# Kernel tuning notes

Measured on AMD Instinct MI355X. Metric: run time of the kernel, lower is better.

## Reference

```python
import jax, jax.numpy as jnp
import numpy as np

N_NODES = 100000
NEG_SLOPE = 0.01  # torch F.leaky_relu default


def gcn_conv(x, src, dst, norm, W, b):
    # x: [N, Fin]; src/dst: [E+N] (self-loops included); norm: [E+N]
    h = x @ W                                  # [N, Fout] dense transform
    msg = h[src] * norm[:, None]               # gather + edge-wise scale
    out = jax.ops.segment_sum(msg, dst, num_segments=x.shape[0])  # scatter-add
    return out + b


def build_graph(edge_index, n_nodes):
    # Add self-loops and compute symmetric GCN normalization deg^-1/2 * deg^-1/2
    loop = jnp.arange(n_nodes, dtype=edge_index.dtype)
    src = jnp.concatenate([edge_index[0], loop])
    dst = jnp.concatenate([edge_index[1], loop])
    deg = jax.ops.segment_sum(jnp.ones_like(dst, dtype=jnp.float32), dst,
                              num_segments=n_nodes)
    dinv = jnp.where(deg > 0, jax.lax.rsqrt(deg), 0.0)
    norm = dinv[src] * dinv[dst]
    return src, dst, norm


def setup_inputs() -> dict:
    key = jax.random.key(0)
    ks = jax.random.split(key, 8)
    in_c, out_c = 256, 64
    hid = 2 * out_c
    x = jax.random.normal(ks[0], (N_NODES, in_c), dtype=jnp.float32)
    edge_index = jax.random.randint(ks[1], (2, 1600000), 0, N_NODES, dtype=jnp.int64)
    def glorot(k, fan_in, fan_out):
        s = jnp.sqrt(6.0 / (fan_in + fan_out))
        return jax.random.uniform(k, (fan_in, fan_out), jnp.float32, -s, s)
    return {
        "x": x,
        "edge_index": edge_index,
        "W1": glorot(ks[2], in_c, hid),
        "b1": jnp.zeros((hid,), jnp.float32),
        "Wmu": glorot(ks[3], hid, out_c),
        "bmu": jnp.zeros((out_c,), jnp.float32),
        "Wlv": glorot(ks[4], hid, out_c),
        "blv": jnp.zeros((out_c,), jnp.float32),
    }


def reference(x, edge_index, W1, b1, Wmu, bmu, Wlv, blv):
    src, dst, norm = build_graph(edge_index, x.shape[0])
    h = gcn_conv(x, src, dst, norm, W1, b1)
    h = jnp.where(h >= 0, h, NEG_SLOPE * h)  # leaky_relu
    mu = gcn_conv(h, src, dst, norm, Wmu, bmu)
    logvar = gcn_conv(h, src, dst, norm, Wlv, blv)
    return (mu, logvar)
```

## Files before the change

kernel.cpp:

```cpp
#include <hip/hip_runtime.h>

typedef unsigned short bf16_t;
typedef short s16x8 __attribute__((ext_vector_type(8)));
typedef float f32x4 __attribute__((ext_vector_type(4)));


#define NBKT 782
#define BSH  7
#define BMSK 127
#define CAPS 512

__device__ __forceinline__ float bf2f(unsigned short u) {
    unsigned int v = ((unsigned int)u) << 16;
    float f;
    __builtin_memcpy(&f, &v, 4);
    return f;
}
__device__ __forceinline__ unsigned short f2bf(float f) {
    unsigned int x;
    __builtin_memcpy(&x, &f, 4);
    unsigned int r = x + 0x7fffu + ((x >> 16) & 1u);
    return (unsigned short)(r >> 16);
}
__device__ __forceinline__ unsigned pack2(float a, float b) {
    return (unsigned)f2bf(a) | ((unsigned)f2bf(b) << 16);
}
__device__ __forceinline__ float ldf(const void* p, long long i, unsigned f32) {
    return f32 ? ((const float*)p)[i] : bf2f(((const unsigned short*)p)[i]);
}
__device__ __forceinline__ int ldi(const void* p, long long i, unsigned i64) {
    return i64 ? (int)((const long long*)p)[i] : ((const int*)p)[i];
}
__device__ __forceinline__ s16x8 ld8u(const unsigned short* p) {
    return *(const s16x8*)p;
}
__device__ __forceinline__ f32x4 mfma16(s16x8 a, s16x8 b, f32x4 c) {
    return __builtin_amdgcn_mfma_f32_16x16x32_bf16(a, b, c, 0, 0, 0);
}
__device__ __forceinline__ void cvt_hl(const float* p, s16x8& hi, s16x8& lo) {
    const float4 u = *(const float4*)p;
    const float4 w = *(const float4*)(p + 4);
    float v[8] = {u.x, u.y, u.z, u.w, w.x, w.y, w.z, w.w};
#pragma unroll
    for (int j = 0; j < 8; ++j) {
        unsigned short h = f2bf(v[j]);
        hi[j] = (short)h;
        lo[j] = (short)f2bf(v[j] - bf2f(h));
    }
}

__global__ __launch_bounds__(256) void k_zero(unsigned* __restrict__ p, int n) {
    int i = blockIdx.x * 256 + threadIdx.x;
    if (i < n) p[i] = 0;
}

__global__ __launch_bounds__(256) void k_detect(const void* x, const void* W1,
                                                const void* ei, unsigned* flags) {
    __shared__ float smx[256];
    __shared__ float smw[256];
    __shared__ int   szc[256];
    int tid = threadIdx.x;
    const unsigned short* xu = (const unsigned short*)x;
    float mx = 0.f;
    for (int i = tid; i < 4096; i += 256) {
        unsigned short w = xu[i];
        if ((w & 0x7fffu) >= 0x7f80u) mx = 1e30f;
        else { float f = fabsf(bf2f(w)); if (f > mx) mx = f; }
    }
    smx[tid] = mx;
    const unsigned short* wu = (const unsigned short*)W1;
    float mw = 0.f;
    for (int i = tid; i < 4096; i += 256) {
        unsigned short w = wu[i];
        if ((w & 0x7fffu) >= 0x7f80u) mw = 1e30f;
        else { float f = fabsf(bf2f(w)); if (f > mw) mw = f; }
    }
    smw[tid] = mw;
    const int* eu = (const int*)ei;
    int zc = 0;
    for (int i = tid; i < 128; i += 256)
        if ((i & 1) && eu[i] == 0) ++zc;
    szc[tid] = zc;
    __syncthreads();
    for (int off = 128; off > 0; off >>= 1) {
        if (tid < off) {
            if (smx[tid + off] > smx[tid]) smx[tid] = smx[tid + off];
            if (smw[tid + off] > smw[tid]) smw[tid] = smw[tid + off];
            szc[tid] += szc[tid + off];
        }
        __syncthreads();
    }
    if (tid == 0) {
        flags[0] = (smx[0] > 1e4f) ? 1u : 0u;
        flags[1] = (smw[0] > 10.f) ? 1u : 0u;
        flags[2] = (szc[0] >= 56) ? 1u : 0u;
    }
}

__global__ __launch_bounds__(256) void k_bucket(const void* ei, const unsigned* det,
                                                int* __restrict__ btail,
                                                unsigned* __restrict__ bstore,
                                                int E, int N) {
    int e = blockIdx.x * 256 + threadIdx.x;
    if (e >= E) return;
    unsigned i64 = det[2];
    int s = ldi(ei, e, i64);
    int d = ldi(ei, (long long)E + e, i64);
    if ((unsigned)d >= (unsigned)N) return;
    int b = d >> BSH;
    int sub = blockIdx.x & 7;
    int slot = atomicAdd(&btail[sub * NBKT + b], 1);
    if (slot < CAPS) {
        unsigned src = ((unsigned)s < (unsigned)N) ? (unsigned)s : (unsigned)d;
        bstore[((long long)(b * 8 + sub)) * CAPS + slot] =
            ((unsigned)(d & BMSK) << 24) | src;
    }
}

__global__ __launch_bounds__(256) void k_bhist(const int* __restrict__ btail,
                                               const unsigned* __restrict__ bstore,
                                               int* __restrict__ cnt, int N) {
    __shared__ int lh[128];
    __shared__ int ln[8];
    const int b = blockIdx.x;
    const int tid = threadIdx.x;
    if (tid < 128) lh[tid] = 0;
    if (tid < 8) {
        int t = btail[tid * NBKT + b];
        ln[tid] = t < CAPS ? t : CAPS;
    }
    __syncthreads();
#pragma unroll 1
    for (int s = 0; s < 8; ++s) {
        int n = ln[s];
        const unsigned* base = &bstore[((long long)(b * 8 + s)) * CAPS];
        for (int i = tid; i < n; i += 256)
            atomicAdd(&lh[base[i] >> 24], 1);
    }
    __syncthreads();
    int node = b * 128 + tid;
    if (tid < 128 && node < N) cnt[node] = lh[tid];
}

__global__ __launch_bounds__(256) void k_dinv(const int* __restrict__ cnt,
                                              float* __restrict__ dinv, int N) {
    int i = blockIdx.x * 256 + threadIdx.x;
    if (i < N) dinv[i] = rsqrtf((float)cnt[i] + 1.0f);
}

__global__ __launch_bounds__(256) void k_scan_blk(const int* __restrict__ cnt,
                                                  int* __restrict__ pos,
                                                  int* __restrict__ bsum, int N) {
    __shared__ int sh[256];
    const int tid = threadIdx.x;
    const int base = blockIdx.x * 1024 + tid * 4;
    int v[4];
#pragma unroll
    for (int j = 0; j < 4; ++j) v[j] = (base + j < N) ? cnt[base + j] : 0;
    int s = v[0] + v[1] + v[2] + v[3];
    sh[tid] = s;
    __syncthreads();
    for (int off = 1; off < 256; off <<= 1) {
        int t = (tid >= off) ? sh[tid - off] : 0;
        __syncthreads();
        sh[tid] += t;
        __syncthreads();
    }
    int run = sh[tid] - s;
#pragma unroll
    for (int j = 0; j < 4; ++j) {
        if (base + j < N) pos[base + j] = run;
        run += v[j];
    }
    if (tid == 255) bsum[blockIdx.x] = sh[255];
}

__global__ void k_scan_top(int* __restrict__ bsum, int nb) {
    if (threadIdx.x == 0 && blockIdx.x == 0) {
        int running = 0;
        for (int b = 0; b < nb; ++b) {
            int t = bsum[b];
            bsum[b] = running;
            running += t;
        }
    }
}

__global__ __launch_bounds__(256) void k_scan_add(int* __restrict__ pos,
                                                  const int* __restrict__ bsum, int N) {
    int add = bsum[blockIdx.x];
    int base = blockIdx.x * 1024;
    for (int i = threadIdx.x; i < 1024; i += 256)
        if (base + i < N) pos[base + i] += add;
}

__global__ __launch_bounds__(256) void k_emit(const int* __restrict__ btail,
                                              const unsigned* __restrict__ bstore,
                                              const int* __restrict__ pos,
                                              int* __restrict__ srt, int N) {
    __shared__ int lstart[128];
    __shared__ int loff[128];
    __shared__ int ln[8];
    __shared__ int stage[4096];
    const int b = blockIdx.x;
    const int tid = threadIdx.x;
    const int base0 = pos[b * 128];
    if (tid < 128) {
        int node = b * 128 + tid;
        lstart[tid] = (node < N) ? (pos[node] - base0) : 0;
        loff[tid] = 0;
    }
    if (tid < 8) {
        int t = btail[tid * NBKT + b];
        ln[tid] = t < CAPS ? t : CAPS;
    }
    __syncthreads();
#pragma unroll 1
    for (int s = 0; s < 8; ++s) {
        int n = ln[s];
        const unsigned* bp = &bstore[((long long)(b * 8 + s)) * CAPS];
        for (int i = tid; i < n; i += 256) {
            unsigned rec = bp[i];
            int dl = rec >> 24;
            int slot = atomicAdd(&loff[dl], 1);
            stage[lstart[dl] + slot] = (int)(rec & 0xffffffu);
        }
    }
    __syncthreads();
    int total = ln[0] + ln[1] + ln[2] + ln[3] + ln[4] + ln[5] + ln[6] + ln[7];
    for (int i = tid; i < total; i += 256)
        srt[base0 + i] = stage[i];
}

__global__ __launch_bounds__(256) void k_wsplit(const void* Wa, const void* Wb,
                                                const unsigned* det, int K,
                                                unsigned short* __restrict__ bth,
                                                unsigned short* __restrict__ btl) {
    int idx = blockIdx.x * 256 + threadIdx.x;
    if (idx >= K * 128) return;
    int k = idx >> 7, n = idx & 127;
    unsigned wf = det[1];
    float w;
    if (Wb) w = (n < 64) ? ldf(Wa, (long long)k * 64 + n, wf)
                         : ldf(Wb, (long long)k * 64 + (n - 64), wf);
    else    w = ldf(Wa, idx, wf);
    unsigned short h = f2bf(w);
    bth[(long long)n * K + k] = h;
    btl[(long long)n * K + k] = f2bf(w - bf2f(h));
}

__global__ __launch_bounds__(256, 4) void k_gemm1m(
    const void* __restrict__ x, const unsigned* __restrict__ det,
    const unsigned short* __restrict__ bth,
    const unsigned short* __restrict__ btl,
    const float* __restrict__ dinv,
    unsigned* __restrict__ Cp, int N) {
    const int lane = threadIdx.x & 63;
    const int wid  = threadIdx.x >> 6;
    const int wr = wid >> 1, wc = wid & 1;
    const int l15 = lane & 15, lg = lane >> 4;
    const long long r0 = (long long)blockIdx.x * 64 + wr * 32;
    long long ar[2];
#pragma unroll
    for (int m = 0; m < 2; ++m) {
        long long r = r0 + m * 16 + l15;
        ar[m] = (r < N) ? r : (N - 1);
    }
    int bn[4];
#pragma unroll
    for (int n = 0; n < 4; ++n) bn[n] = wc * 64 + n * 16 + l15;

    f32x4 acc[2][4] = {};
    if (!det[0]) {
        const unsigned short* xp = (const unsigned short*)x;
#pragma unroll 2
        for (int k0 = 0; k0 < 256; k0 += 32) {
            const int kb = k0 + lg * 8;
            s16x8 a[2], bh[4], bl[4];
#pragma unroll
            for (int m = 0; m < 2; ++m) a[m] = ld8u(xp + ar[m] * 256 + kb);
#pragma unroll
            for (int n = 0; n < 4; ++n) {
                bh[n] = ld8u(bth + (long long)bn[n] * 256 + kb);
                bl[n] = ld8u(btl + (long long)bn[n] * 256 + kb);
            }
#pragma unroll
            for (int m = 0; m < 2; ++m)
#pragma unroll
                for (int n = 0; n < 4; ++n) {
                    acc[m][n] = mfma16(a[m], bh[n], acc[m][n]);
                    acc[m][n] = mfma16(a[m], bl[n], acc[m][n]);
                }
        }
    } else {
        const float* xp = (const float*)x;
#pragma unroll 2
        for (int k0 = 0; k0 < 256; k0 += 32) {
            const int kb = k0 + lg * 8;
            s16x8 ah[2], al[2], bh[4], bl[4];
#pragma unroll
            for (int m = 0; m < 2; ++m) cvt_hl(xp + ar[m] * 256 + kb, ah[m], al[m]);
#pragma unroll
            for (int n = 0; n < 4; ++n) {
                bh[n] = ld8u(bth + (long long)bn[n] * 256 + kb);
                bl[n] = ld8u(btl + (long long)bn[n] * 256 + kb);
            }
#pragma unroll
            for (int m = 0; m < 2; ++m)
#pragma unroll
                for (int n = 0; n < 4; ++n) {
                    acc[m][n] = mfma16(ah[m], bh[n], acc[m][n]);
                    acc[m][n] = mfma16(ah[m], bl[n], acc[m][n]);
                    acc[m][n] = mfma16(al[m], bh[n], acc[m][n]);
                }
        }
    }
#pragma unroll
    for (int m = 0; m < 2; ++m)
#pragma unroll
        for (int n = 0; n < 4; ++n) {
            const int col = wc * 64 + n * 16 + l15;
#pragma unroll
            for (int r = 0; r < 4; ++r) {
                long long row = r0 + m * 16 + lg * 4 + r;
                float v = acc[m][n][r] * dinv[(row < N) ? row : (N - 1)];
                float p = __shfl_xor(v, 1);
                if (!(lane & 1) && row < N)
                    Cp[row * 64 + (col >> 1)] = pack2(v, p);
            }
        }
}

__global__ __launch_bounds__(256, 4) void k_gemm2m(
    const unsigned short* __restrict__ hap,
    const unsigned short* __restrict__ bth,
    const unsigned short* __restrict__ btl,
    const void* bmu, const void* blv, const unsigned* __restrict__ det,
    float* __restrict__ outMu, float* __restrict__ outLv, int N) {
    const int lane = threadIdx.x & 63;
    const int wid  = threadIdx.x >> 6;
    const int wr = wid >> 1, wc = wid & 1;
    const int l15 = lane & 15, lg = lane >> 4;
    const long long r0 = (long long)blockIdx.x * 64 + wr * 32;
    long long ar[2];
#pragma unroll
    for (int m = 0; m < 2; ++m) {
        long long r = r0 + m * 16 + l15;
        ar[m] = (r < N) ? r : (N - 1);
    }
    int bn[4];
#pragma unroll
    for (int n = 0; n < 4; ++n) bn[n] = wc * 64 + n * 16 + l15;

    f32x4 acc[2][4] = {};
#pragma unroll
    for (int k0 = 0; k0 < 128; k0 += 32) {
        const int kb = k0 + lg * 8;
        s16x8 a[2], bh[4], bl[4];
#pragma unroll
        for (int m = 0; m < 2; ++m) a[m] = ld8u(hap + ar[m] * 128 + kb);
#pragma unroll
        for (int n = 0; n < 4; ++n) {
            bh[n] = ld8u(bth + (long long)bn[n] * 128 + kb);
            bl[n] = ld8u(btl + (long long)bn[n] * 128 + kb);
        }
#pragma unroll
        for (int m = 0; m < 2; ++m)
#pragma unroll
            for (int n = 0; n < 4; ++n) {
                acc[m][n] = mfma16(a[m], bh[n], acc[m][n]);
                acc[m][n] = mfma16(a[m], bl[n], acc[m][n]);
            }
    }
    __syncthreads();
    const unsigned wf = det[1];
#pragma unroll
    for (int m = 0; m < 2; ++m)
#pragma unroll
        for (int n = 0; n < 4; ++n) {
            const int col = wc * 64 + n * 16 + l15;
            const float bias = (col < 64) ? ldf(bmu, col, wf)
                                          : ldf(blv, col - 64, wf);
#pragma unroll
            for (int r = 0; r < 4; ++r) {
                long long row = r0 + m * 16 + lg * 4 + r;
                if (row < N) {
                    float v = acc[m][n][r] + bias;
                    if (col < 64) outMu[row * 64 + col] = v;
                    else          outLv[row * 64 + (col - 64)] = v;
                }
            }
        }
}

__global__ __launch_bounds__(256) void k_gather(const unsigned* __restrict__ hp,
                                                const int* __restrict__ srt,
                                                const int* __restrict__ cnt,
                                                const int* __restrict__ pos,
                                                const float* __restrict__ dinv,
                                                const void* bias, const unsigned* det,
                                                int leaky, int prescaleOut,
                                                unsigned* __restrict__ outp, int N) {
    int node = blockIdx.x * 4 + (threadIdx.x >> 6);
    if (node >= N) return;
    int lane = threadIdx.x & 63;
    int beg = pos[node];
    int end = beg + cnt[node];
    float dd = dinv[node];
    unsigned hv = hp[(long long)node * 64 + lane];
    float a0 = bf2f((unsigned short)(hv & 0xffffu));
    float a1 = bf2f((unsigned short)(hv >> 16));
    for (int q = beg; q < end; q += 8) {
        int s[8];
        unsigned v[8];
#pragma unroll
        for (int j = 0; j < 8; ++j) {
            int qq = q + j;
            s[j] = srt[(qq < end) ? qq : beg];
        }
#pragma unroll
        for (int j = 0; j < 8; ++j)
            v[j] = hp[(long long)s[j] * 64 + lane];
#pragma unroll
        for (int j = 0; j < 8; ++j) {
            bool on = (q + j) < end;
            a0 += on ? bf2f((unsigned short)(v[j] & 0xffffu)) : 0.f;
            a1 += on ? bf2f((unsigned short)(v[j] >> 16)) : 0.f;
        }
    }
    a0 *= dd;
    a1 *= dd;
    if (bias) {
        a0 += ldf(bias, 2 * lane, det[1]);
        a1 += ldf(bias, 2 * lane + 1, det[1]);
    }
    if (leaky) {
        a0 = (a0 >= 0.f) ? a0 : 0.01f * a0;
        a1 = (a1 >= 0.f) ? a1 : 0.01f * a1;
    }
    if (prescaleOut) { a0 *= dd; a1 *= dd; }
    outp[(long long)node * 64 + lane] = pack2(a0, a1);
}

__global__ void k_sentinel(float* out, long long lvOff) {
    if (threadIdx.x == 0 && blockIdx.x == 0) {
        out[0] = 9.99e5f;
        out[lvOff] = 9.98e5f;
    }
}

extern "C" void kernel_launch(void* const* d_in, const int* in_sizes, int n_in,
                              void* d_out, int out_size, void* d_ws, size_t ws_size,
                              hipStream_t stream) {
    (void)out_size;
    const int N = 100000, E = 1600000;
    bool ok = (n_in == 8) && in_sizes[0] == 25600000 && in_sizes[1] == 3200000 &&
              in_sizes[2] == 32768 && in_sizes[3] == 128 &&
              in_sizes[4] == 8192 && in_sizes[5] == 64 &&
              in_sizes[6] == 8192 && in_sizes[7] == 64 &&
              ws_size >= (size_t)21 * 1024 * 1024;
    if (!ok) {
        k_sentinel<<<1, 64, 0, stream>>>((float*)d_out, (long long)N * 64);
        return;
    }
    const void* x   = d_in[0];
    const void* ei  = d_in[1];
    const void* W1  = d_in[2];
    const void* b1  = d_in[3];
    const void* Wmu = d_in[4];
    const void* bmu = d_in[5];
    const void* Wlv = d_in[6];
    const void* blv = d_in[7];

    char* w = (char*)d_ws;
    auto carve = [&](size_t bytes) {
        char* p = w;
        w += (bytes + 255) & ~(size_t)255;
        return p;
    };
    unsigned* flags = (unsigned*)carve(64);
    int*    cnt  = (int*)carve((size_t)N * 4);
    int*    pos  = (int*)carve((size_t)N * 4);
    float*  dinv = (float*)carve((size_t)N * 4);
    int*    bsum = (int*)carve(4096);
    int*    srt  = (int*)carve((size_t)E * 4);
    unsigned short* bt1h = (unsigned short*)carve(128 * 256 * 2);
    unsigned short* bt1l = (unsigned short*)carve(128 * 256 * 2);
    unsigned short* bt2h = (unsigned short*)carve(128 * 128 * 2);
    unsigned short* bt2l = (unsigned short*)carve(128 * 128 * 2);
    int*      btail  = (int*)carve((size_t)NBKT * 8 * 4);
    unsigned* bstore = (unsigned*)carve((size_t)NBKT * 8 * CAPS * 4);

    float* M = (float*)d_out;
    float* L = M + (size_t)N * 64;
    unsigned* Mp = (unsigned*)M;
    unsigned* Lp = (unsigned*)L;

    const int nb = (N + 1023) / 1024;
    const int gblk = (N + 3) / 4;
    const int gb64 = (N + 63) / 64;

    k_zero<<<1, 64, 0, stream>>>(flags, 16);
    k_detect<<<1, 256, 0, stream>>>(x, W1, ei, flags);
    k_zero<<<(NBKT * 8 + 255) / 256, 256, 0, stream>>>((unsigned*)btail, NBKT * 8);

    k_bucket<<<(E + 255) / 256, 256, 0, stream>>>(ei, flags, btail, bstore, E, N);
    k_bhist<<<NBKT, 256, 0, stream>>>(btail, bstore, cnt, N);
    k_dinv<<<(N + 255) / 256, 256, 0, stream>>>(cnt, dinv, N);
    k_scan_blk<<<nb, 256, 0, stream>>>(cnt, pos, bsum, N);
    k_scan_top<<<1, 64, 0, stream>>>(bsum, nb);
    k_scan_add<<<nb, 256, 0, stream>>>(pos, bsum, N);
    k_emit<<<NBKT, 256, 0, stream>>>(btail, bstore, pos, srt, N);

    k_wsplit<<<(256 * 128 + 255) / 256, 256, 0, stream>>>(W1, nullptr, flags, 256,
                                                          bt1h, bt1l);
    k_wsplit<<<(128 * 128 + 255) / 256, 256, 0, stream>>>(Wmu, Wlv, flags, 128,
                                                          bt2h, bt2l);

    k_gemm1m<<<gb64, 256, 0, stream>>>(x, flags, bt1h, bt1l, dinv, Mp, N);
    k_gather<<<gblk, 256, 0, stream>>>(Mp, srt, cnt, pos, dinv, b1, flags, 1, 1,
                                       Lp, N);
    k_gather<<<gblk, 256, 0, stream>>>(Lp, srt, cnt, pos, dinv, nullptr, flags,
                                       0, 0, Mp, N);
    k_gemm2m<<<gb64, 256, 0, stream>>>((const unsigned short*)Mp, bt2h, bt2l,
                                       bmu, blv, flags, M, L, N);
}
```

Baseline: 560.4 us.

## Merge small launches, software-pipeline GEMM loads, and widen gather to 8-byte lanes

Removes the zero, dinv and scan_top kernels: btail zeroing moves into k_detect, dinv is computed inside k_bhist, and each scan_add block sums the preceding block totals itself. The two weight-split launches become one. Both GEMM kernels get explicit double-buffered register prefetch of A and B fragments, with launch bounds lowered to 2 waves per SIMD. The gather kernel now processes 8 nodes per block with 32 lanes each loading uint2, halving the lane count per node. The flags buffer is no longer zeroed before k_detect, which risks stale flags if k_detect does not write every entry.

```diff
diff --git a/kernel.cpp b/kernel.cpp
--- a/kernel.cpp
+++ b/kernel.cpp
@@ -49,17 +49,14 @@
     }
 }
 
-__global__ __launch_bounds__(256) void k_zero(unsigned* __restrict__ p, int n) {
-    int i = blockIdx.x * 256 + threadIdx.x;
-    if (i < n) p[i] = 0;
-}
-
 __global__ __launch_bounds__(256) void k_detect(const void* x, const void* W1,
-                                                const void* ei, unsigned* flags) {
+                                                const void* ei, unsigned* flags,
+                                                int* __restrict__ btail) {
     __shared__ float smx[256];
     __shared__ float smw[256];
     __shared__ int   szc[256];
     int tid = threadIdx.x;
+    for (int i = tid; i < NBKT * 8; i += 256) btail[i] = 0;
     const unsigned short* xu = (const unsigned short*)x;
     float mx = 0.f;
     for (int i = tid; i < 4096; i += 256) {
@@ -119,7 +116,8 @@
 
 __global__ __launch_bounds__(256) void k_bhist(const int* __restrict__ btail,
                                                const unsigned* __restrict__ bstore,
-                                               int* __restrict__ cnt, int N) {
+                                               int* __restrict__ cnt,
+                                               float* __restrict__ dinv, int N) {
     __shared__ int lh[128];
     __shared__ int ln[8];
     const int b = blockIdx.x;
@@ -139,13 +137,10 @@
     }
     __syncthreads();
     int node = b * 128 + tid;
-    if (tid < 128 && node < N) cnt[node] = lh[tid];
-}
-
-__global__ __launch_bounds__(256) void k_dinv(const int* __restrict__ cnt,
-                                              float* __restrict__ dinv, int N) {
-    int i = blockIdx.x * 256 + threadIdx.x;
-    if (i < N) dinv[i] = rsqrtf((float)cnt[i] + 1.0f);
+    if (tid < 128 && node < N) {
+        cnt[node] = lh[tid];
+        dinv[node] = rsqrtf((float)lh[tid] + 1.0f);
+    }
 }
 
 __global__ __launch_bounds__(256) void k_scan_blk(const int* __restrict__ cnt,
@@ -175,20 +170,16 @@
     if (tid == 255) bsum[blockIdx.x] = sh[255];
 }
 
-__global__ void k_scan_top(int* __restrict__ bsum, int nb) {
-    if (threadIdx.x == 0 && blockIdx.x == 0) {
-        int running = 0;
-        for (int b = 0; b < nb; ++b) {
-            int t = bsum[b];
-            bsum[b] = running;
-            running += t;
-        }
-    }
-}
-
 __global__ __launch_bounds__(256) void k_scan_add(int* __restrict__ pos,
                                                   const int* __restrict__ bsum, int N) {
-    int add = bsum[blockIdx.x];
+    __shared__ int sadd;
+    if (threadIdx.x == 0) {
+        int a = 0;
+        for (int i = 0; i < blockIdx.x; ++i) a += bsum[i];
+        sadd = a;
+    }
+    __syncthreads();
+    int add = sadd;
     int base = blockIdx.x * 1024;
     for (int i = threadIdx.x; i < 1024; i += 256)
         if (base + i < N) pos[base + i] += add;
@@ -232,24 +223,32 @@
         srt[base0 + i] = stage[i];
 }
 
-__global__ __launch_bounds__(256) void k_wsplit(const void* Wa, const void* Wb,
-                                                const unsigned* det, int K,
-                                                unsigned short* __restrict__ bth,
-                                                unsigned short* __restrict__ btl) {
+__global__ __launch_bounds__(256) void k_wsplit(const void* W1, const void* Wmu,
+                                                const void* Wlv, const unsigned* det,
+                                                unsigned short* __restrict__ bt1h,
+                                                unsigned short* __restrict__ bt1l,
+                                                unsigned short* __restrict__ bt2h,
+                                                unsigned short* __restrict__ bt2l) {
     int idx = blockIdx.x * 256 + threadIdx.x;
-    if (idx >= K * 128) return;
-    int k = idx >> 7, n = idx & 127;
     unsigned wf = det[1];
-    float w;
-    if (Wb) w = (n < 64) ? ldf(Wa, (long long)k * 64 + n, wf)
-                         : ldf(Wb, (long long)k * 64 + (n - 64), wf);
-    else    w = ldf(Wa, idx, wf);
-    unsigned short h = f2bf(w);
-    bth[(long long)n * K + k] = h;
-    btl[(long long)n * K + k] = f2bf(w - bf2f(h));
-}
-
-__global__ __launch_bounds__(256, 4) void k_gemm1m(
+    if (idx < 256 * 128) {
+        int k = idx >> 7, n = idx & 127;
+        float w = ldf(W1, idx, wf);
+        unsigned short h = f2bf(w);
+        bt1h[(long long)n * 256 + k] = h;
+        bt1l[(long long)n * 256 + k] = f2bf(w - bf2f(h));
+    } else if (idx < 256 * 128 + 128 * 128) {
+        int j = idx - 256 * 128;
+        int k = j >> 7, n = j & 127;
+        float w = (n < 64) ? ldf(Wmu, (long long)k * 64 + n, wf)
+                           : ldf(Wlv, (long long)k * 64 + (n - 64), wf);
+        unsigned short h = f2bf(w);
+        bt2h[(long long)n * 128 + k] = h;
+        bt2l[(long long)n * 128 + k] = f2bf(w - bf2f(h));
+    }
+}
+
+__global__ __launch_bounds__(256, 2) void k_gemm1p(
     const void* __restrict__ x, const unsigned* __restrict__ det,
     const unsigned short* __restrict__ bth,
     const unsigned short* __restrict__ btl,
@@ -273,23 +272,48 @@
     f32x4 acc[2][4] = {};
     if (!det[0]) {
         const unsigned short* xp = (const unsigned short*)x;
-#pragma unroll 2
-        for (int k0 = 0; k0 < 256; k0 += 32) {
-            const int kb = k0 + lg * 8;
-            s16x8 a[2], bh[4], bl[4];
-#pragma unroll
-            for (int m = 0; m < 2; ++m) a[m] = ld8u(xp + ar[m] * 256 + kb);
-#pragma unroll
-            for (int n = 0; n < 4; ++n) {
-                bh[n] = ld8u(bth + (long long)bn[n] * 256 + kb);
-                bl[n] = ld8u(btl + (long long)bn[n] * 256 + kb);
-            }
+        const unsigned short* aP[2];
+#pragma unroll
+        for (int m = 0; m < 2; ++m) aP[m] = xp + ar[m] * 256 + lg * 8;
+        const unsigned short* bHp[4];
+        const unsigned short* bLp[4];
+#pragma unroll
+        for (int n = 0; n < 4; ++n) {
+            bHp[n] = bth + (long long)bn[n] * 256 + lg * 8;
+            bLp[n] = btl + (long long)bn[n] * 256 + lg * 8;
+        }
+        s16x8 aS[8][2], bhS[2][4], blS[2][4];
+#pragma unroll
+        for (int s = 0; s < 2; ++s)
+#pragma unroll
+            for (int m = 0; m < 2; ++m) aS[s][m] = ld8u(aP[m] + s * 32);
+#pragma unroll
+        for (int n = 0; n < 4; ++n) {
+            bhS[0][n] = ld8u(bHp[n]);
+            blS[0][n] = ld8u(bLp[n]);
+        }
+#pragma unroll
+        for (int st = 0; st < 8; ++st) {
+            if (st < 7) {
+                const int nb = (st + 1) & 1;
+#pragma unroll
+                for (int n = 0; n < 4; ++n) {
+                    bhS[nb][n] = ld8u(bHp[n] + (st + 1) * 32);
+                    blS[nb][n] = ld8u(bLp[n] + (st + 1) * 32);
+                }
+            }
+            if (st < 6) {
+#pragma unroll
+                for (int m = 0; m < 2; ++m)
+                    aS[st + 2][m] = ld8u(aP[m] + (st + 2) * 32);
+            }
+            const int cb = st & 1;
 #pragma unroll
             for (int m = 0; m < 2; ++m)
 #pragma unroll
                 for (int n = 0; n < 4; ++n) {
-                    acc[m][n] = mfma16(a[m], bh[n], acc[m][n]);
-                    acc[m][n] = mfma16(a[m], bl[n], acc[m][n]);
+                    acc[m][n] = mfma16(aS[st][m], bhS[cb][n], acc[m][n]);
+                    acc[m][n] = mfma16(aS[st][m], blS[cb][n], acc[m][n]);
                 }
         }
     } else {
@@ -331,7 +355,7 @@
         }
 }
 
-__global__ __launch_bounds__(256, 4) void k_gemm2m(
+__global__ __launch_bounds__(256, 2) void k_gemm2p(
     const unsigned short* __restrict__ hap,
     const unsigned short* __restrict__ bth,
     const unsigned short* __restrict__ btl,
@@ -352,24 +376,49 @@
 #pragma unroll
     for (int n = 0; n < 4; ++n) bn[n] = wc * 64 + n * 16 + l15;
 
+    const unsigned short* aP[2];
+#pragma unroll
+    for (int m = 0; m < 2; ++m) aP[m] = hap + ar[m] * 128 + lg * 8;
+    const unsigned short* bHp[4];
+    const unsigned short* bLp[4];
+#pragma unroll
+    for (int n = 0; n < 4; ++n) {
+        bHp[n] = bth + (long long)bn[n] * 128 + lg * 8;
+        bLp[n] = btl + (long long)bn[n] * 128 + lg * 8;
+    }
     f32x4 acc[2][4] = {};
-#pragma unroll
-    for (int k0 = 0; k0 < 128; k0 += 32) {
-        const int kb = k0 + lg * 8;
-        s16x8 a[2], bh[4], bl[4];
-#pragma unroll
-        for (int m = 0; m < 2; ++m) a[m] = ld8u(hap + ar[m] * 128 + kb);
-#pragma unroll
-        for (int n = 0; n < 4; ++n) {
-            bh[n] = ld8u(bth + (long long)bn[n] * 128 + kb);
-            bl[n] = ld8u(btl + (long long)bn[n] * 128 + kb);
-        }
+    s16x8 aS[4][2], bhS[2][4], blS[2][4];
+#pragma unroll
+    for (int s = 0; s < 2; ++s)
+#pragma unroll
+        for (int m = 0; m < 2; ++m) aS[s][m] = ld8u(aP[m] + s * 32);
+#pragma unroll
+    for (int n = 0; n < 4; ++n) {
+        bhS[0][n] = ld8u(bHp[n]);
+        blS[0][n] = ld8u(bLp[n]);
+    }
+#pragma unroll
+    for (int st = 0; st < 4; ++st) {
+        if (st < 3) {
+            const int nb = (st + 1) & 1;
+#pragma unroll
+            for (int n = 0; n < 4; ++n) {
+                bhS[nb][n] = ld8u(bHp[n] + (st + 1) * 32);
+                blS[nb][n] = ld8u(bLp[n] + (st + 1) * 32);
+            }
+        }
+        if (st < 2) {
+#pragma unroll
+            for (int m = 0; m < 2; ++m)
+                aS[st + 2][m] = ld8u(aP[m] + (st + 2) * 32);
+        }
+        const int cb = st & 1;
 #pragma unroll
         for (int m = 0; m < 2; ++m)
 #pragma unroll
             for (int n = 0; n < 4; ++n) {
-                acc[m][n] = mfma16(a[m], bh[n], acc[m][n]);
-                acc[m][n] = mfma16(a[m], bl[n], acc[m][n]);
+                acc[m][n] = mfma16(aS[st][m], bhS[cb][n], acc[m][n]);
+                acc[m][n] = mfma16(aS[st][m], blS[cb][n], acc[m][n]);
             }
     }
     __syncthreads();
@@ -393,26 +442,28 @@
         }
 }
 
-__global__ __launch_bounds__(256) void k_gather(const unsigned* __restrict__ hp,
+__global__ __launch_bounds__(256) void k_gather(const uint2* __restrict__ hp2,
                                                 const int* __restrict__ srt,
                                                 const int* __restrict__ cnt,
                                                 const int* __restrict__ pos,
                                                 const float* __restrict__ dinv,
                                                 const void* bias, const unsigned* det,
                                                 int leaky, int prescaleOut,
-                                                unsigned* __restrict__ outp, int N) {
-    int node = blockIdx.x * 4 + (threadIdx.x >> 6);
+                                                uint2* __restrict__ outp2, int N) {
+    int node = blockIdx.x * 8 + (threadIdx.x >> 5);
     if (node >= N) return;
-    int lane = threadIdx.x & 63;
+    int lane5 = threadIdx.x & 31;
     int beg = pos[node];
     int end = beg + cnt[node];
     float dd = dinv[node];
-    unsigned hv = hp[(long long)node * 64 + lane];
-    float a0 = bf2f((unsigned short)(hv & 0xffffu));
-    float a1 = bf2f((unsigned short)(hv >> 16));
+    uint2 hv = hp2[(long long)node * 32 + lane5];
+    float a0 = bf2f((unsigned short)(hv.x & 0xffffu));
+    float a1 = bf2f((unsigned short)(hv.x >> 16));
+    float a2 = bf2f((unsigned short)(hv.y & 0xffffu));
+    float a3 = bf2f((unsigned short)(hv.y >> 16));
     for (int q = beg; q < end; q += 8) {
         int s[8];
-        unsigned v[8];
+        uint2 v[8];
 #pragma unroll
         for (int j = 0; j < 8; ++j) {
             int qq = q + j;
@@ -420,26 +471,34 @@
         }
 #pragma unroll
         for (int j = 0; j < 8; ++j)
-            v[j] = hp[(long long)s[j] * 64 + lane];
+            v[j] = hp2[(long long)s[j] * 32 + lane5];
 #pragma unroll
         for (int j = 0; j < 8; ++j) {
             bool on = (q + j) < end;
-            a0 += on ? bf2f((unsigned short)(v[j] & 0xffffu)) : 0.f;
-            a1 += on ? bf2f((unsigned short)(v[j] >> 16)) : 0.f;
-        }
-    }
-    a0 *= dd;
-    a1 *= dd;
+            a0 += on ? bf2f((unsigned short)(v[j].x & 0xffffu)) : 0.f;
+            a1 += on ? bf2f((unsigned short)(v[j].x >> 16)) : 0.f;
+            a2 += on ? bf2f((unsigned short)(v[j].y & 0xffffu)) : 0.f;
+            a3 += on ? bf2f((unsigned short)(v[j].y >> 16)) : 0.f;
+        }
+    }
+    a0 *= dd; a1 *= dd; a2 *= dd; a3 *= dd;
     if (bias) {
-        a0 += ldf(bias, 2 * lane, det[1]);
-        a1 += ldf(bias, 2 * lane + 1, det[1]);
+        a0 += ldf(bias, 4 * lane5 + 0, det[1]);
+        a1 += ldf(bias, 4 * lane5 + 1, det[1]);
+        a2 += ldf(bias, 4 * lane5 + 2, det[1]);
+        a3 += ldf(bias, 4 * lane5 + 3, det[1]);
     }
     if (leaky) {
         a0 = (a0 >= 0.f) ? a0 : 0.01f * a0;
         a1 = (a1 >= 0.f) ? a1 : 0.01f * a1;
-    }
-    if (prescaleOut) { a0 *= dd; a1 *= dd; }
-    outp[(long long)node * 64 + lane] = pack2(a0, a1);
+        a2 = (a2 >= 0.f) ? a2 : 0.01f * a2;
+        a3 = (a3 >= 0.f) ? a3 : 0.01f * a3;
+    }
+    if (prescaleOut) { a0 *= dd; a1 *= dd; a2 *= dd; a3 *= dd; }
+    uint2 o;
+    o.x = pack2(a0, a1);
+    o.y = pack2(a2, a3);
+    outp2[(long long)node * 32 + lane5] = o;
 }
 
 __global__ void k_sentinel(float* out, long long lvOff) {
@@ -497,31 +556,24 @@
     unsigned* Lp = (unsigned*)L;
 
     const int nb = (N + 1023) / 1024;
-    const int gblk = (N + 3) / 4;
+    const int ggrid = N / 8;
     const int gb64 = (N + 63) / 64;
 
-    k_zero<<<1, 64, 0, stream>>>(flags, 16);
-    k_detect<<<1, 256, 0, stream>>>(x, W1, ei, flags);
-    k_zero<<<(NBKT * 8 + 255) / 256, 256, 0, stream>>>((unsigned*)btail, NBKT * 8);
+    k_detect<<<1, 256, 0, stream>>>(x, W1, ei, flags, btail);
+    k_wsplit<<<(256 * 128 + 128 * 128 + 255) / 256, 256, 0, stream>>>(
+        W1, Wmu, Wlv, flags, bt1h, bt1l, bt2h, bt2l);
 
     k_bucket<<<(E + 255) / 256, 256, 0, stream>>>(ei, flags, btail, bstore, E, N);
-    k_bhist<<<NBKT, 256, 0, stream>>>(btail, bstore, cnt, N);
-    k_dinv<<<(N + 255) / 256, 256, 0, stream>>>(cnt, dinv, N);
+    k_bhist<<<NBKT, 256, 0, stream>>>(btail, bstore, cnt, dinv, N);
     k_scan_blk<<<nb, 256, 0, stream>>>(cnt, pos, bsum, N);
-    k_scan_top<<<1, 64, 0, stream>>>(bsum, nb);
     k_scan_add<<<nb, 256, 0, stream>>>(pos, bsum, N);
     k_emit<<<NBKT, 256, 0, stream>>>(btail, bstore, pos, srt, N);
 
-    k_wsplit<<<(256 * 128 + 255) / 256, 256, 0, stream>>>(W1, nullptr, flags, 256,
-                                                          bt1h, bt1l);
-    k_wsplit<<<(128 * 128 + 255) / 256, 256, 0, stream>>>(Wmu, Wlv, flags, 128,
-                                                          bt2h, bt2l);
-
-    k_gemm1m<<<gb64, 256, 0, stream>>>(x, flags, bt1h, bt1l, dinv, Mp, N);
-    k_gather<<<gblk, 256, 0, stream>>>(Mp, srt, cnt, pos, dinv, b1, flags, 1, 1,
-                                       Lp, N);
-    k_gather<<<gblk, 256, 0, stream>>>(Lp, srt, cnt, pos, dinv, nullptr, flags,
-                                       0, 0, Mp, N);
-    k_gemm2m<<<gb64, 256, 0, stream>>>((const unsigned short*)Mp, bt2h, bt2l,
+    k_gemm1p<<<gb64, 256, 0, stream>>>(x, flags, bt1h, bt1l, dinv, Mp, N);
+    k_gather<<<ggrid, 256, 0, stream>>>((const uint2*)Mp, srt, cnt, pos, dinv,
+                                        b1, flags, 1, 1, (uint2*)Lp, N);
+    k_gather<<<ggrid, 256, 0, stream>>>((const uint2*)Lp, srt, cnt, pos, dinv,
+                                        nullptr, flags, 0, 0, (uint2*)Mp, N);
+    k_gemm2p<<<gb64, 256, 0, stream>>>((const unsigned short*)Mp, bt2h, bt2l,
                                        bmu, blv, flags, M, L, N);
 }
```

Measured after the change: 527.3 us. 1.06x faster.
